# Optimization experiments

Measured on AMD Instinct MI355X. Metric: run time of the kernel, lower is better.

## Reference

```python
import jax, jax.numpy as jnp
import numpy as np
import math
from jax import lax

N_SCALES = 5
ORDER = 2
INC, OUTC = 20, 40
MIN = np.arange(N_SCALES) * 0.2          # per-scale band lower edges [0,.2,.4,.6,.8]
MAX = MIN + 0.2                          # per-scale band upper edges [.2,...,1.0]
SIGMA0 = (MIN + MAX) / 2.0               # sigma at init (scales=0 -> tanh=0)
FS = [int(math.ceil(2.0 * s)) for s in SIGMA0]  # static half filter sizes [1,1,1,2,2]
MAXK = 2 * max(FS) + 1                   # padded kernel size (5)


def _hermite_derivs(x, sigma, order):
    # n-th Gaussian derivative: (-1/(sigma*sqrt2))^n * H_n(x/(sigma*sqrt2)) * g(x)
    g = jnp.exp(-(x ** 2) / (2.0 * sigma ** 2))
    g = g / jnp.sum(g)  # unit-sum normalized Gaussian envelope
    u = x / (sigma * math.sqrt(2.0))
    H = [jnp.ones_like(u), 2.0 * u]
    for n in range(1, order):
        H.append(2.0 * u * H[n] - 2.0 * n * H[n - 1])
    return [((-1.0 / (sigma * math.sqrt(2.0))) ** n) * H[n] * g for n in range(order + 1)]


def _basis(x, sigma, order):
    # 2D separable Gaussian-Hermite basis, all (i,j) with i+j <= order -> [N,k,k]
    d = _hermite_derivs(x, sigma, order)
    return jnp.stack([jnp.outer(d[i], d[j])
                      for i in range(order + 1) for j in range(order + 1 - i)])


def _make_filters(alphas, scales):
    mn = jnp.asarray(MIN, jnp.float32)
    mx = jnp.asarray(MAX, jnp.float32)
    sigma = (mx - mn) / 2.0 * jnp.tanh(scales) + (mn + mx) / 2.0  # learn_sigma=True path
    filts = []
    for s in range(N_SCALES):
        x = jnp.arange(-FS[s], FS[s] + 1, dtype=jnp.float32)
        B = _basis(x, sigma[s], ORDER)                    # [N, k, k]
        f = jnp.einsum('nkl,nio->oikl', B, alphas[s])     # [outC/ns, inC/ns, k, k]
        p = (MAXK - (2 * FS[s] + 1)) // 2                 # zero-pad to common size
        f = jnp.pad(f, ((0, 0), (0, 0), (p, p), (p, p)))
        filts.append(f)
    return jnp.concatenate(filts, axis=0)                 # [outC, inC/ns, K, K]


def setup_inputs() -> dict:
    key = jax.random.key(0)
    k1, k2 = jax.random.split(key)
    n_basis = (ORDER + 1) * (ORDER + 2) // 2  # 6
    data = jax.random.normal(k1, (16, INC, 384, 384), dtype=jnp.float32)
    alphas = jax.random.normal(k2, (N_SCALES, n_basis, INC // N_SCALES, OUTC // N_SCALES), dtype=jnp.float32)
    scales = jnp.zeros((N_SCALES,), dtype=jnp.float32)
    return {"data": data, "alphas": alphas, "scales": scales}


def reference(data, alphas, scales):
    w = _make_filters(alphas, scales)
    pad = MAXK // 2
    return lax.conv_general_dilated(
        data, w, window_strides=(1, 1), padding=[(pad, pad), (pad, pad)],
        dimension_numbers=('NCHW', 'OIHW', 'NCHW'),
        feature_group_count=N_SCALES)
```

## Files before the change

### kernel.cpp

```cpp
#include <hip/hip_runtime.h>
#include <hip/hip_bf16.h>
#include <math.h>

#define BATCH 16
#define G 5
#define CI 4
#define CO 8
#define HW 384
#define KK 5
#define PADD 2


__global__ void gen_weights(const float* __restrict__ alphas,
                            const float* __restrict__ scales,
                            float* __restrict__ w) {
    int idx = blockIdx.x * blockDim.x + threadIdx.x;
    if (idx >= G * CI * KK * KK) return;
    int kx = idx % 5; int r = idx / 5;
    int ky = r % 5;   r /= 5;
    int i  = r % 4;   int s = r / 4;

    float mn = 0.2f * (float)s;
    float mx = mn + 0.2f;
    float sigma = 0.5f * (mx - mn) * tanhf(scales[s]) + 0.5f * (mn + mx);
    int fs = (s < 3) ? 1 : 2;
    int p  = 2 - fs;

    float outw[CO];
    bool valid = (ky >= p) && (ky < 5 - p) && (kx >= p) && (kx < 5 - p);
    if (!valid) {
        #pragma unroll
        for (int o = 0; o < CO; ++o) outw[o] = 0.f;
    } else {
        float inv2s2 = 1.f / (2.f * sigma * sigma);
        float Gs = 0.f;
        for (int t = -fs; t <= fs; ++t) Gs += expf(-(float)(t * t) * inv2s2);
        const float sqrt2 = 1.41421356237309505f;
        float c = -1.f / (sigma * sqrt2);

        float xy = (float)(ky - p - fs);
        float xx = (float)(kx - p - fs);

        float gy = expf(-xy * xy * inv2s2) / Gs;
        float gx = expf(-xx * xx * inv2s2) / Gs;
        float uy = xy / (sigma * sqrt2);
        float ux = xx / (sigma * sqrt2);

        float dy[3], dx[3];
        dy[0] = gy;
        dy[1] = c * 2.f * uy * gy;
        dy[2] = c * c * (4.f * uy * uy - 2.f) * gy;
        dx[0] = gx;
        dx[1] = c * 2.f * ux * gx;
        dx[2] = c * c * (4.f * ux * ux - 2.f) * gx;

        float bas[6];
        bas[0] = dy[0] * dx[0];
        bas[1] = dy[0] * dx[1];
        bas[2] = dy[0] * dx[2];
        bas[3] = dy[1] * dx[0];
        bas[4] = dy[1] * dx[1];
        bas[5] = dy[2] * dx[0];

        #pragma unroll
        for (int o = 0; o < CO; ++o) {
            float acc = 0.f;
            #pragma unroll
            for (int n = 0; n < 6; ++n)
                acc += bas[n] * alphas[((s * 6 + n) * CI + i) * CO + o];
            outw[o] = acc;
        }
    }
    float* dst = w + ((((s * CI + i) * KK + ky) * KK + kx) * CO);
    #pragma unroll
    for (int o = 0; o < CO; ++o) dst[o] = outw[o];
}

#define TLE 32
#define IT 36

typedef float v2f __attribute__((ext_vector_type(2)));

__global__ __launch_bounds__(256) void conv_kernel(const float* __restrict__ in,
                                                   const float* __restrict__ w,
                                                   float* __restrict__ out) {
    __shared__ float s_in[CI][IT][IT];
    __shared__ float s_w[CI * KK * KK * CO];

    const int tileX = blockIdx.x * TLE;
    const int tileY = blockIdx.y * TLE;
    const int bz = blockIdx.z;
    const int g = bz % G;
    const int b = bz / G;
    const int tid = threadIdx.x;

    const float* wg = w + g * (CI * KK * KK * CO);
    for (int l = tid; l < CI * KK * KK * CO; l += 256) s_w[l] = wg[l];

    const float* inb = in + ((size_t)b * (G * CI) + g * CI) * (HW * HW);
    for (int l = tid; l < CI * IT * IT; l += 256) {
        int c = l / (IT * IT);
        int r = l - c * (IT * IT);
        int ly = r / IT;
        int lx = r - ly * IT;
        int gy = tileY - PADD + ly;
        int gx = tileX - PADD + lx;
        float v = 0.f;
        if ((unsigned)gy < (unsigned)HW && (unsigned)gx < (unsigned)HW)
            v = inb[c * (HW * HW) + gy * HW + gx];
        s_in[c][ly][lx] = v;
    }
    __syncthreads();

    const int xc = tid & 7;
    const int ty = tid >> 3;
    const int xl0 = xc * 4;

    v2f acc[CO][2];
    #pragma unroll
    for (int o = 0; o < CO; ++o) { acc[o][0] = (v2f)0.f; acc[o][1] = (v2f)0.f; }

    for (int i = 0; i < CI; ++i) {
        #pragma unroll
        for (int ky = 0; ky < KK; ++ky) {
            const float* row = &s_in[i][ty + ky][xl0];
            float4 a0 = *(const float4*)(row);
            float4 a1 = *(const float4*)(row + 4);
            float  a8 = row[8];
            float iv[9] = {a0.x, a0.y, a0.z, a0.w, a1.x, a1.y, a1.z, a1.w, a8};
            const float* wrow = &s_w[(i * (KK * KK) + ky * KK) * CO];
            #pragma unroll
            for (int kx = 0; kx < KK; ++kx) {
                float4 w0 = *(const float4*)(wrow + kx * CO);
                float4 w1 = *(const float4*)(wrow + kx * CO + 4);
                v2f v01 = {iv[kx],     iv[kx + 1]};
                v2f v23 = {iv[kx + 2], iv[kx + 3]};
                float wv[8] = {w0.x, w0.y, w0.z, w0.w, w1.x, w1.y, w1.z, w1.w};
                #pragma unroll
                for (int o = 0; o < CO; ++o) {
                    v2f ws = {wv[o], wv[o]};
                    acc[o][0] += ws * v01;
                    acc[o][1] += ws * v23;
                }
            }
        }
    }

    const int oy = tileY + ty;
    float* outb = out + (((size_t)b * (G * CO) + g * CO) * HW + oy) * HW + tileX + xl0;
    #pragma unroll
    for (int o = 0; o < CO; ++o) {
        float4 rr;
        rr.x = acc[o][0][0];
        rr.y = acc[o][0][1];
        rr.z = acc[o][1][0];
        rr.w = acc[o][1][1];
        *(float4*)(outb + (size_t)o * (HW * HW)) = rr;
    }
}

extern "C" void kernel_launch(void* const* d_in, const int* in_sizes, int n_in,
                              void* d_out, int out_size, void* d_ws, size_t ws_size,
                              hipStream_t stream) {
    const float* data   = (const float*)d_in[0];
    const float* alphas = (const float*)d_in[1];
    const float* scales = (const float*)d_in[2];
    float* out = (float*)d_out;
    float* w   = (float*)d_ws;

    gen_weights<<<2, 256, 0, stream>>>(alphas, scales, w);

    dim3 grid(HW / TLE, HW / TLE, BATCH * G);
    conv_kernel<<<grid, 256, 0, stream>>>(data, w, out);
}
```

Baseline: 669.8 us.

## Remap threads to per-output-channel 4x8 pixel tiles with register-blocked inputs

Each thread now computes a 4x8 pixel block for a single output channel instead of a 1x4 strip across all eight channels. It loads an 8x12 input window and its 25 weights into registers, which raises input reuse from registers. The shared-memory weight layout is transposed to [oc][ci][28] so that weights load as float4, and the input tile row stride is padded to 40. The trade-off is higher register pressure from 96 input registers plus 32 accumulators, and output stores now go to different rows per thread.

Result: slower. 853.2 us (+27.4%).

```diff
diff --git a/kernel.cpp b/kernel.cpp
--- a/kernel.cpp
+++ b/kernel.cpp
@@ -77,15 +77,14 @@
 }
 
 #define TLE 32
-#define IT 36
-
-typedef float v2f __attribute__((ext_vector_type(2)));
+#define ITY 36
+#define SSTR 40
 
 __global__ __launch_bounds__(256) void conv_kernel(const float* __restrict__ in,
                                                    const float* __restrict__ w,
                                                    float* __restrict__ out) {
-    __shared__ float s_in[CI][IT][IT];
-    __shared__ float s_w[CI * KK * KK * CO];
+    __shared__ float s_in[CI][ITY][SSTR];
+    __shared__ float s_w[CO][CI][28];
 
     const int tileX = blockIdx.x * TLE;
     const int tileY = blockIdx.y * TLE;
@@ -95,14 +94,20 @@
     const int tid = threadIdx.x;
 
     const float* wg = w + g * (CI * KK * KK * CO);
-    for (int l = tid; l < CI * KK * KK * CO; l += 256) s_w[l] = wg[l];
+    for (int l = tid; l < CI * KK * KK * CO; l += 256) {
+        int oc = l & 7;
+        int r = l >> 3;
+        int i = r / 25;
+        int k = r - i * 25;
+        s_w[oc][i][k] = wg[(i * 25 + k) * CO + oc];
+    }
 
     const float* inb = in + ((size_t)b * (G * CI) + g * CI) * (HW * HW);
-    for (int l = tid; l < CI * IT * IT; l += 256) {
-        int c = l / (IT * IT);
-        int r = l - c * (IT * IT);
-        int ly = r / IT;
-        int lx = r - ly * IT;
+    for (int l = tid; l < CI * 36 * 36; l += 256) {
+        int c = l / (36 * 36);
+        int r = l - c * (36 * 36);
+        int ly = r / 36;
+        int lx = r - ly * 36;
         int gy = tileY - PADD + ly;
         int gx = tileX - PADD + lx;
         float v = 0.f;
@@ -112,50 +117,63 @@
     }
     __syncthreads();
 
-    const int xc = tid & 7;
-    const int ty = tid >> 3;
-    const int xl0 = xc * 4;
+    const int oc  = tid & 7;
+    const int pix = tid >> 3;
+    const int yb  = pix >> 2;
+    const int xc  = pix & 3;
+    const int ty0 = yb * 4;
+    const int xl0 = xc * 8;
 
-    v2f acc[CO][2];
+    float acc[4][8];
     #pragma unroll
-    for (int o = 0; o < CO; ++o) { acc[o][0] = (v2f)0.f; acc[o][1] = (v2f)0.f; }
+    for (int oy = 0; oy < 4; ++oy)
+        #pragma unroll
+        for (int x = 0; x < 8; ++x) acc[oy][x] = 0.f;
 
     for (int i = 0; i < CI; ++i) {
+        float rbuf[8][12];
+        #pragma unroll
+        for (int rr = 0; rr < 8; ++rr) {
+            const float* p = &s_in[i][ty0 + rr][xl0];
+            float4 a = *(const float4*)(p);
+            float4 bq = *(const float4*)(p + 4);
+            float4 cq = *(const float4*)(p + 8);
+            rbuf[rr][0] = a.x;  rbuf[rr][1] = a.y;  rbuf[rr][2]  = a.z;  rbuf[rr][3]  = a.w;
+            rbuf[rr][4] = bq.x; rbuf[rr][5] = bq.y; rbuf[rr][6]  = bq.z; rbuf[rr][7]  = bq.w;
+            rbuf[rr][8] = cq.x; rbuf[rr][9] = cq.y; rbuf[rr][10] = cq.z; rbuf[rr][11] = cq.w;
+        }
+        float wv[28];
+        #pragma unroll
+        for (int q = 0; q < 7; ++q) {
+            float4 t = *(const float4*)(&s_w[oc][i][4 * q]);
+            wv[4 * q + 0] = t.x; wv[4 * q + 1] = t.y;
+            wv[4 * q + 2] = t.z; wv[4 * q + 3] = t.w;
+        }
+
         #pragma unroll
         for (int ky = 0; ky < KK; ++ky) {
-            const float* row = &s_in[i][ty + ky][xl0];
-            float4 a0 = *(const float4*)(row);
-            float4 a1 = *(const float4*)(row + 4);
-            float  a8 = row[8];
-            float iv[9] = {a0.x, a0.y, a0.z, a0.w, a1.x, a1.y, a1.z, a1.w, a8};
-            const float* wrow = &s_w[(i * (KK * KK) + ky * KK) * CO];
             #pragma unroll
-            for (int kx = 0; kx < KK; ++kx) {
-                float4 w0 = *(const float4*)(wrow + kx * CO);
-                float4 w1 = *(const float4*)(wrow + kx * CO + 4);
-                v2f v01 = {iv[kx],     iv[kx + 1]};
-                v2f v23 = {iv[kx + 2], iv[kx + 3]};
-                float wv[8] = {w0.x, w0.y, w0.z, w0.w, w1.x, w1.y, w1.z, w1.w};
+            for (int oy = 0; oy < 4; ++oy) {
                 #pragma unroll
-                for (int o = 0; o < CO; ++o) {
-                    v2f ws = {wv[o], wv[o]};
-                    acc[o][0] += ws * v01;
-                    acc[o][1] += ws * v23;
+                for (int kx = 0; kx < KK; ++kx) {
+                    float wgt = wv[ky * 5 + kx];
+                    #pragma unroll
+                    for (int x = 0; x < 8; ++x)
+                        acc[oy][x] = fmaf(wgt, rbuf[oy + ky][kx + x], acc[oy][x]);
                 }
             }
         }
     }
 
-    const int oy = tileY + ty;
-    float* outb = out + (((size_t)b * (G * CO) + g * CO) * HW + oy) * HW + tileX + xl0;
+    const int oy0 = tileY + ty0;
+    float* outb = out + (((size_t)b * (G * CO) + (size_t)g * CO + oc) * HW + oy0) * HW + tileX + xl0;
     #pragma unroll
-    for (int o = 0; o < CO; ++o) {
-        float4 rr;
-        rr.x = acc[o][0][0];
-        rr.y = acc[o][0][1];
-        rr.z = acc[o][1][0];
-        rr.w = acc[o][1][1];
-        *(float4*)(outb + (size_t)o * (HW * HW)) = rr;
+    for (int oy = 0; oy < 4; ++oy) {
+        float4 r0, r1;
+        r0.x = acc[oy][0]; r0.y = acc[oy][1]; r0.z = acc[oy][2]; r0.w = acc[oy][3];
+        r1.x = acc[oy][4]; r1.y = acc[oy][5]; r1.z = acc[oy][6]; r1.w = acc[oy][7];
+        *(float4*)(outb + (size_t)oy * HW) = r0;
+        *(float4*)(outb + (size_t)oy * HW + 4) = r1;
     }
 }
 
```
